# Optimization experiments

Hardware: AMD Instinct MI355X
Metric: run time of the kernel (lower is better)

The kernel has to match this reference:

```python
import jax, jax.numpy as jnp
import numpy as np

NH, NL, NP = 8, 4, 4  # heads, levels, points per head per level
SHAPES = [(100, 134), (50, 67), (25, 34), (13, 17)]  # (H, W) per level, strides 8/16/32/64


def rms_norm(x, w, eps=1e-6):
    return x * jax.lax.rsqrt(jnp.mean(x * x, axis=-1, keepdims=True) + eps) * w


def bilinear_sample(value_l, loc, H, W):
    """grid_sample(bilinear, zeros padding, align_corners=False) equivalent.
    value_l: (bs, nh, H*W, d); loc: (bs, Lq, nh, P, 2) normalized to [0,1].
    Returns (bs, Lq, nh, P, d)."""
    bs, Lq, nh, P, _ = loc.shape
    x = loc[..., 0] * W - 0.5
    y = loc[..., 1] * H - 0.5
    x0 = jnp.floor(x); y0 = jnp.floor(y)
    lx = x - x0; ly = y - y0
    x0i = x0.astype(jnp.int32); y0i = y0.astype(jnp.int32)
    out = None
    for dy, dx in ((0, 0), (0, 1), (1, 0), (1, 1)):
        wgt = (lx if dx else 1.0 - lx) * (ly if dy else 1.0 - ly)
        xi = x0i + dx; yi = y0i + dy
        valid = (xi >= 0) & (xi < W) & (yi >= 0) & (yi < H)
        idx = jnp.clip(yi, 0, H - 1) * W + jnp.clip(xi, 0, W - 1)  # (bs,Lq,nh,P)
        idx_t = idx.transpose(0, 2, 1, 3).reshape(bs, nh, Lq * P)
        g = jnp.take_along_axis(value_l, idx_t[..., None], axis=2)  # (bs,nh,Lq*P,d)
        g = g.reshape(bs, nh, Lq, P, -1).transpose(0, 2, 1, 3, 4)    # (bs,Lq,nh,P,d)
        term = g * (wgt * valid)[..., None]
        out = term if out is None else out + term
    return out


def _forward(query, query_pos, reference_points, norm_attn_w, Wv, bv, Woff, boff, Waw, baw, Wo, bo, ls_attn_g, norm_ffn_w, W1, b1, W2, b2, W3, b3, ls_ffn_g):
    bs, Lq, C = query.shape
    d = C // NH
    # --- pre-norm MSDeformAttn with identity=0 (LayerScale residual applied outside) ---
    normed = rms_norm(query, norm_attn_w)
    q = normed + query_pos  # query_pos only affects offsets/weights, not value
    value = (normed @ Wv.T + bv).reshape(bs, Lq, NH, d).transpose(0, 2, 1, 3)  # (bs,nh,Nv,d)
    off = (q @ Woff.T + boff).reshape(bs, Lq, NH, NL, NP, 2)
    aw = jax.nn.softmax((q @ Waw.T + baw).reshape(bs, Lq, NH, NL * NP), axis=-1)
    aw = aw.reshape(bs, Lq, NH, NL, NP)
    normalizer = jnp.array([[w, h] for (h, w) in SHAPES], dtype=query.dtype)  # (NL,2) = (W,H)
    loc = reference_points[:, :, None, :, None, :] + off / normalizer[None, None, None, :, None, :]
    out = jnp.zeros((bs, Lq, NH, d), query.dtype)
    start = 0
    for l, (H, W) in enumerate(SHAPES):
        v_l = jax.lax.dynamic_slice_in_dim(value, start, H * W, axis=2)
        samp = bilinear_sample(v_l, loc[:, :, :, l], H, W)  # (bs,Lq,nh,P,d)
        out = out + jnp.einsum('bqhpd,bqhp->bqhd', samp, aw[:, :, :, l])
        start += H * W
    attn_out = out.reshape(bs, Lq, C) @ Wo.T + bo
    x = query + ls_attn_g * attn_out
    # --- pre-norm SwiGLU FFN with LayerScale residual ---
    n2 = rms_norm(x, norm_ffn_w)
    h = jax.nn.silu(n2 @ W1.T + b1) * (n2 @ W2.T + b2)
    return x + ls_ffn_g * (h @ W3.T + b3)


def setup_inputs() -> dict:
    key = jax.random.key(0)
    ks = jax.random.split(key, 12)
    bs, C, dffn = 2, 256, 1024
    Lq = sum(h * w for h, w in SHAPES)  # 17821
    p = 0.02
    return {
        'query': jax.random.normal(ks[0], (bs, Lq, C), jnp.float32),
        'query_pos': jax.random.normal(ks[1], (bs, Lq, C), jnp.float32),
        'reference_points': jax.random.uniform(ks[2], (bs, Lq, NL, 2), jnp.float32),
        'spatial_shapes': jnp.array(SHAPES, jnp.int32),
        'level_start_index': jnp.array(np.cumsum([0] + [h * w for h, w in SHAPES])[:-1], jnp.int32),
        'norm_attn_w': jnp.ones((C,), jnp.float32),
        'Wv': jax.random.normal(ks[3], (C, C), jnp.float32) * p,
        'bv': jnp.zeros((C,), jnp.float32),
        'Woff': jax.random.normal(ks[4], (NH * NL * NP * 2, C), jnp.float32) * p,
        'boff': jax.random.uniform(ks[5], (NH * NL * NP * 2,), jnp.float32, -1.0, 1.0),
        'Waw': jax.random.normal(ks[6], (NH * NL * NP, C), jnp.float32) * p,
        'baw': jnp.zeros((NH * NL * NP,), jnp.float32),
        'Wo': jax.random.normal(ks[7], (C, C), jnp.float32) * p,
        'bo': jnp.zeros((C,), jnp.float32),
        'ls_attn_g': jnp.full((C,), 1e-4, jnp.float32),
        'norm_ffn_w': jnp.ones((C,), jnp.float32),
        'W1': jax.random.normal(ks[8], (dffn, C), jnp.float32) * p,
        'b1': jnp.zeros((dffn,), jnp.float32),
        'W2': jax.random.normal(ks[9], (dffn, C), jnp.float32) * p,
        'b2': jnp.zeros((dffn,), jnp.float32),
        'W3': jax.random.normal(ks[10], (C, dffn), jnp.float32) * p,
        'b3': jnp.zeros((C,), jnp.float32),
        'ls_ffn_g': jnp.full((C,), 1e-4, jnp.float32),
    }


def reference(query, query_pos, reference_points, spatial_shapes, level_start_index, norm_attn_w, Wv, bv, Woff, boff, Waw, baw, Wo, bo, ls_attn_g, norm_ffn_w, W1, b1, W2, b2, W3, b3, ls_ffn_g):
    del spatial_shapes, level_start_index  # static shapes baked into SHAPES
    return _forward(query, query_pos, reference_points, norm_attn_w, Wv, bv, Woff, boff, Waw, baw, Wo, bo, ls_attn_g, norm_ffn_w, W1, b1, W2, b2, W3, b3, ls_ffn_g)
```

## Files before the change

### kernel.cpp

```cpp
#include <hip/hip_runtime.h>
#include <hip/hip_bf16.h>
#include <cstddef>

#define LQ   17821
#define BS   2
#define MTOK (BS * LQ)
#define CDIM 256
#define NHD  8
#define DHEAD 32
#define DFFN 1024

typedef short bf16x4 __attribute__((ext_vector_type(4)));
typedef short bf16x8 __attribute__((ext_vector_type(8)));
typedef float f32x4  __attribute__((ext_vector_type(4)));
typedef float f32x2  __attribute__((ext_vector_type(2)));

__device__ __forceinline__ unsigned char fp8_enc(float f) {
#if __has_builtin(__builtin_amdgcn_cvt_pk_fp8_f32)
    return (unsigned char)(__builtin_amdgcn_cvt_pk_fp8_f32(f, f, 0, false) & 0xff);
#else
    unsigned s = (__float_as_uint(f) >> 31) << 7;
    float af = fabsf(f);
    if (af < 0.0078125f) return (unsigned char)s;
    af = fminf(af, 448.f);
    unsigned b = __float_as_uint(af);
    int e = (int)(b >> 23) - 127 + 7;
    unsigned m = (b >> 20) & 7;
    if (b & 0x80000) { m++; if (m == 8) { m = 0; e++; } }
    if (e < 1) return (unsigned char)s;
    if (e > 15) { e = 15; m = 6; }
    return (unsigned char)(s | ((unsigned)e << 3) | m);
#endif
}

__device__ __forceinline__ float fp8_dec_byte(unsigned x) {
    unsigned s = (x >> 7) & 1, e = (x >> 3) & 15, m = x & 7;
    float v = e ? __uint_as_float(((e + 120u) << 23) | (m << 20))
                : (float)m * 0.001953125f;
    return s ? -v : v;
}

template <bool HI>
__device__ __forceinline__ f32x2 fp8_dec2(unsigned d) {
#if __has_builtin(__builtin_amdgcn_cvt_pk_f32_fp8)
    return __builtin_amdgcn_cvt_pk_f32_fp8(d, HI);
#else
    f32x2 r;
    r[0] = fp8_dec_byte((d >> (HI ? 16 : 0)) & 0xff);
    r[1] = fp8_dec_byte((d >> (HI ? 24 : 8)) & 0xff);
    return r;
#endif
}

__device__ __forceinline__ ushort bfpack(float f) {
    __hip_bfloat16 h = (__hip_bfloat16)f;
    return *(ushort*)&h;
}

__device__ __forceinline__ void stage_a8(short* p, uint2 d) {
    const f32x2 p0 = fp8_dec2<false>(d.x), p1 = fp8_dec2<true>(d.x);
    const f32x2 p2 = fp8_dec2<false>(d.y), p3 = fp8_dec2<true>(d.y);
    bf16x4 lo, hi;
    lo[0] = (short)bfpack(p0[0]); lo[1] = (short)bfpack(p0[1]);
    lo[2] = (short)bfpack(p1[0]); lo[3] = (short)bfpack(p1[1]);
    hi[0] = (short)bfpack(p2[0]); hi[1] = (short)bfpack(p2[1]);
    hi[2] = (short)bfpack(p3[0]); hi[3] = (short)bfpack(p3[1]);
    ((bf16x4*)p)[0] = lo;
    ((bf16x4*)p)[1] = hi;
}

struct CastJobs {
    const float* src[7];
    __hip_bfloat16* dst[7];
    const float* colw[7];
    int n[7];
};

__global__ __launch_bounds__(256)
void cast_all(CastJobs j) {
    const int seg = blockIdx.y;
    const int i = blockIdx.x * 256 + threadIdx.x;
    if (i < j.n[seg]) {
        float v = j.src[seg][i];
        if (j.colw[seg]) v *= j.colw[seg][i & 255];
        j.dst[seg][i] = (__hip_bfloat16)v;
    }
}

template <bool ADD_POS>
__global__ __launch_bounds__(256)
void rmsnorm_kernel(const float* __restrict__ x, const float* __restrict__ pos,
                    const float* __restrict__ w,
                    __hip_bfloat16* __restrict__ outN, __hip_bfloat16* __restrict__ outQ) {
    const int tok = blockIdx.x * 4 + (threadIdx.x >> 6);
    if (tok >= MTOK) return;
    const int lane = threadIdx.x & 63;
    const size_t base = (size_t)tok * CDIM + lane * 4;
    const float4 v = *(const float4*)&x[base];
    float ss = v.x * v.x + v.y * v.y + v.z * v.z + v.w * v.w;
#pragma unroll
    for (int m = 1; m < 64; m <<= 1) ss += __shfl_xor(ss, m, 64);
    const float r = rsqrtf(ss * (1.0f / CDIM) + 1e-6f);
    const float4 wv = *(const float4*)&w[lane * 4];
    const float n0 = v.x * r * wv.x, n1 = v.y * r * wv.y;
    const float n2 = v.z * r * wv.z, n3 = v.w * r * wv.w;
    ushort4 o;
    o.x = bfpack(n0); o.y = bfpack(n1); o.z = bfpack(n2); o.w = bfpack(n3);
    *(ushort4*)&outN[base] = o;
    if (ADD_POS) {
        const float4 p = *(const float4*)&pos[base];
        ushort4 q;
        q.x = bfpack(n0 + p.x); q.y = bfpack(n1 + p.y);
        q.z = bfpack(n2 + p.z); q.w = bfpack(n3 + p.w);
        *(ushort4*)&outQ[base] = q;
    }
}

__global__ __launch_bounds__(256)
void rowrms_kernel(const __hip_bfloat16* __restrict__ x, float* __restrict__ r) {
    const int tok = blockIdx.x * 4 + (threadIdx.x >> 6);
    if (tok >= MTOK) return;
    const int lane = threadIdx.x & 63;
    const ushort4 u = *(const ushort4*)&x[(size_t)tok * CDIM + lane * 4];
    const float v0 = __uint_as_float((unsigned)u.x << 16);
    const float v1 = __uint_as_float((unsigned)u.y << 16);
    const float v2 = __uint_as_float((unsigned)u.z << 16);
    const float v3 = __uint_as_float((unsigned)u.w << 16);
    float ss = v0 * v0 + v1 * v1 + v2 * v2 + v3 * v3;
#pragma unroll
    for (int m = 1; m < 64; m <<= 1) ss += __shfl_xor(ss, m, 64);
    if (lane == 0) r[tok] = rsqrtf(ss * (1.0f / CDIM) + 1e-6f);
}

#define GBM 128
#define GBN 128

template <int MODE, int BKT, typename OUTT, bool A8 = false>
__global__ __launch_bounds__(256, 2)
void mfma_gemm(const void* __restrict__ Av,
               const __hip_bfloat16* __restrict__ B1, const float* __restrict__ bias1,
               const float* __restrict__ bias2,
               const float* __restrict__ resid, const __hip_bfloat16* __restrict__ residb,
               const float* __restrict__ ls,
               OUTT* __restrict__ out, int M, int N, int K, int nsw) {
    constexpr int LDKT = BKT + 8;
    constexpr int CH = BKT / 16;
    constexpr int CPR = BKT / 8;

    __shared__ short As[GBM * LDKT];
    __shared__ short Bs[GBN * LDKT];

    const __hip_bfloat16* A = (const __hip_bfloat16*)Av;
    const unsigned char* A8p = (const unsigned char*)Av;

    const int tid = threadIdx.x;
    const int bid = blockIdx.x;
    const int m0 = (bid / nsw) * GBM;
    const int n0 = (bid % nsw) * GBN;
    const int wave = tid >> 6;
    const int lane = tid & 63;
    const int wm = (wave >> 1) * 64;
    const int wn = (wave & 1) * 64;
    const int fr = lane & 15;
    const int fq = lane >> 4;

    f32x4 acc[4][4] = {};

    int srow[CH], skc[CH];
#pragma unroll
    for (int cc = 0; cc < CH; ++cc) {
        const int g = tid + cc * 256;
        srow[cc] = g / CPR;
        skc[cc] = (g % CPR) * 8;
    }
    const uint4 zero4 = make_uint4(0, 0, 0, 0);
    const uint2 zero2 = make_uint2(0, 0);

    uint4 ra[CH], rb[CH];
    uint2 ra8[A8 ? CH : 1];
#pragma unroll
    for (int cc = 0; cc < CH; ++cc) {
        const int gm = m0 + srow[cc];
        if constexpr (A8)
            ra8[cc] = (gm < M) ? *(const uint2*)&A8p[(size_t)gm * K + skc[cc]] : zero2;
        else
            ra[cc] = (gm < M) ? *(const uint4*)&A[(size_t)gm * K + skc[cc]] : zero4;
        rb[cc] = *(const uint4*)&B1[(size_t)(n0 + srow[cc]) * K + skc[cc]];
    }

    for (int k0 = 0; k0 < K; k0 += BKT) {
        __syncthreads();
#pragma unroll
        for (int cc = 0; cc < CH; ++cc) {
            short* pa = &As[srow[cc] * LDKT + skc[cc]];
            short* pb = &Bs[srow[cc] * LDKT + skc[cc]];
            if constexpr (A8) {
                stage_a8(pa, ra8[cc]);
            } else {
                union { uint4 u; bf16x4 h[2]; } cv;
                cv.u = ra[cc]; ((bf16x4*)pa)[0] = cv.h[0]; ((bf16x4*)pa)[1] = cv.h[1];
            }
            union { uint4 u; bf16x4 h[2]; } cv;
            cv.u = rb[cc]; ((bf16x4*)pb)[0] = cv.h[0]; ((bf16x4*)pb)[1] = cv.h[1];
        }
        __syncthreads();

        if (k0 + BKT < K) {
            const int kn = k0 + BKT;
#pragma unroll
            for (int cc = 0; cc < CH; ++cc) {
                const int gm = m0 + srow[cc];
                if constexpr (A8)
                    ra8[cc] = (gm < M) ? *(const uint2*)&A8p[(size_t)gm * K + kn + skc[cc]] : zero2;
                else
                    ra[cc] = (gm < M) ? *(const uint4*)&A[(size_t)gm * K + kn + skc[cc]] : zero4;
                rb[cc] = *(const uint4*)&B1[(size_t)(n0 + srow[cc]) * K + kn + skc[cc]];
            }
        }

#pragma unroll
        for (int kk = 0; kk < BKT; kk += 32) {
            const int kq = kk + fq * 8;
            bf16x8 af[4], bfr[4];
#pragma unroll
            for (int i = 0; i < 4; ++i)
                af[i] = *(const bf16x8*)&As[(wm + i * 16 + fr) * LDKT + kq];
#pragma unroll
            for (int j = 0; j < 4; ++j)
                bfr[j] = *(const bf16x8*)&Bs[(wn + j * 16 + fr) * LDKT + kq];
#pragma unroll
            for (int i = 0; i < 4; ++i)
#pragma unroll
                for (int j = 0; j < 4; ++j)
                    acc[i][j] = __builtin_amdgcn_mfma_f32_16x16x32_bf16(af[i], bfr[j], acc[i][j], 0, 0, 0);
        }
    }

#pragma unroll
    for (int i = 0; i < 4; ++i) {
#pragma unroll
        for (int r = 0; r < 4; ++r) {
            const int m = m0 + wm + i * 16 + fq * 4 + r;
            if (m >= M) continue;
#pragma unroll
            for (int j = 0; j < 4; ++j) {
                const int n = n0 + wn + j * 16 + fr;
                float v;
                if constexpr (MODE == 4)
                    v = acc[i][j][r] + ((n < 256) ? bias1[n] : bias2[n - 256]);
                else
                    v = acc[i][j][r] + bias1[n];
                if constexpr (MODE == 0 || MODE == 4) {
                    out[(size_t)m * N + n] = (OUTT)v;
                } else if constexpr (MODE == 1) {
                    const int b = (m >= LQ) ? 1 : 0;
                    const int qi = m - b * LQ;
                    const int h = n >> 5;
                    const int c = n & 31;
                    ((unsigned char*)out)[((size_t)(b * NHD + h) * LQ + qi) * DHEAD + c] = fp8_enc(v);
                } else if constexpr (MODE == 2) {
                    out[(size_t)m * N + n] =
                        (OUTT)(resid[(size_t)m * N + n] + ls[n] * v);
                } else {
                    const float rx = __uint_as_float(
                        (unsigned)(*(const ushort*)&residb[(size_t)m * N + n]) << 16);
                    out[(size_t)m * N + n] = (OUTT)(rx + ls[n] * v);
                }
            }
        }
    }
}

__global__ __launch_bounds__(256, 3)
void mfma_swiglu(const __hip_bfloat16* __restrict__ A,
                 const __hip_bfloat16* __restrict__ B1, const float* __restrict__ bias1,
                 const __hip_bfloat16* __restrict__ B2, const float* __restrict__ bias2,
                 const float* __restrict__ rrow,
                 unsigned char* __restrict__ out, int M) {
    constexpr int BKT = 32, LDKT = 40, K = CDIM, N = DFFN;
    __shared__ short As[128 * LDKT];
    __shared__ short Bs[64 * LDKT];
    __shared__ short Bs2[64 * LDKT];

    const int tid = threadIdx.x;
    const int bid = blockIdx.x;
    const int m0 = (bid >> 4) * 128;
    const int n0 = (bid & 15) * 64;
    const int wave = tid >> 6;
    const int lane = tid & 63;
    const int wm = (wave >> 1) * 64;
    const int wn = (wave & 1) * 32;
    const int fr = lane & 15;
    const int fq = lane >> 4;

    f32x4 acc[4][2] = {};
    f32x4 acc2[4][2] = {};

    const int arow = tid >> 2;
    const int akc = (tid & 3) * 8;
    const uint4 zero4 = make_uint4(0, 0, 0, 0);

    uint4 ra0, ra1, rb, rc;
    {
        const int gm0 = m0 + arow, gm1 = m0 + arow + 64;
        ra0 = (gm0 < M) ? *(const uint4*)&A[(size_t)gm0 * K + akc] : zero4;
        ra1 = (gm1 < M) ? *(const uint4*)&A[(size_t)gm1 * K + akc] : zero4;
        rb = *(const uint4*)&B1[(size_t)(n0 + arow) * K + akc];
        rc = *(const uint4*)&B2[(size_t)(n0 + arow) * K + akc];
    }

    for (int k0 = 0; k0 < K; k0 += BKT) {
        __syncthreads();
        {
            union { uint4 u; bf16x4 h[2]; } cv;
            short* pa0 = &As[arow * LDKT + akc];
            short* pa1 = &As[(arow + 64) * LDKT + akc];
            short* pb = &Bs[arow * LDKT + akc];
            short* pc = &Bs2[arow * LDKT + akc];
            cv.u = ra0; ((bf16x4*)pa0)[0] = cv.h[0]; ((bf16x4*)pa0)[1] = cv.h[1];
            cv.u = ra1; ((bf16x4*)pa1)[0] = cv.h[0]; ((bf16x4*)pa1)[1] = cv.h[1];
            cv.u = rb;  ((bf16x4*)pb)[0] = cv.h[0]; ((bf16x4*)pb)[1] = cv.h[1];
            cv.u = rc;  ((bf16x4*)pc)[0] = cv.h[0]; ((bf16x4*)pc)[1] = cv.h[1];
        }
        __syncthreads();

        if (k0 + BKT < K) {
            const int kn = k0 + BKT + akc;
            const int gm0 = m0 + arow, gm1 = m0 + arow + 64;
            ra0 = (gm0 < M) ? *(const uint4*)&A[(size_t)gm0 * K + kn] : zero4;
            ra1 = (gm1 < M) ? *(const uint4*)&A[(size_t)gm1 * K + kn] : zero4;
            rb = *(const uint4*)&B1[(size_t)(n0 + arow) * K + kn];
            rc = *(const uint4*)&B2[(size_t)(n0 + arow) * K + kn];
        }

        const int kq = fq * 8;
        bf16x8 af[4], bfr[2], bg[2];
#pragma unroll
        for (int i = 0; i < 4; ++i)
            af[i] = *(const bf16x8*)&As[(wm + i * 16 + fr) * LDKT + kq];
#pragma unroll
        for (int j = 0; j < 2; ++j) {
            bfr[j] = *(const bf16x8*)&Bs[(wn + j * 16 + fr) * LDKT + kq];
            bg[j] = *(const bf16x8*)&Bs2[(wn + j * 16 + fr) * LDKT + kq];
        }
#pragma unroll
        for (int i = 0; i < 4; ++i)
#pragma unroll
            for (int j = 0; j < 2; ++j) {
                acc[i][j] = __builtin_amdgcn_mfma_f32_16x16x32_bf16(af[i], bfr[j], acc[i][j], 0, 0, 0);
                acc2[i][j] = __builtin_amdgcn_mfma_f32_16x16x32_bf16(af[i], bg[j], acc2[i][j], 0, 0, 0);
            }
    }

#pragma unroll
    for (int i = 0; i < 4; ++i) {
#pragma unroll
        for (int r = 0; r < 4; ++r) {
            const int m = m0 + wm + i * 16 + fq * 4 + r;
            if (m >= M) continue;
            const float rm = rrow[m];
#pragma unroll
            for (int j = 0; j < 2; ++j) {
                const int n = n0 + wn + j * 16 + fr;
                const float v1 = acc[i][j][r] * rm + bias1[n];
                const float v2 = acc2[i][j][r] * rm + bias2[n];
                const float sig = 1.0f / (1.0f + expf(-v1));
                out[(size_t)m * N + n] = fp8_enc(v1 * sig * v2);
            }
        }
    }
}

__global__ __launch_bounds__(256)
void sample_kernel(const unsigned char* __restrict__ value,
                   const ushort* __restrict__ proj,
                   const float* __restrict__ ref,
                   __hip_bfloat16* __restrict__ out) {
    __shared__ float wsm[4][NHD][16];
    __shared__ int2  sTap[4][64][9];

    const int tok0 = blockIdx.x * 4;
    const int t = threadIdx.x;

    if (t < 32) {
        const int tl = t >> 3, h = t & 7;
        const int row = tok0 + tl;
        if (row < MTOK) {
            const ushort* lg = &proj[(size_t)row * 384 + 256 + h * 16];
            float v[16];
            float mx = -3.4e38f;
#pragma unroll
            for (int i = 0; i < 16; ++i) {
                v[i] = __uint_as_float((unsigned)lg[i] << 16);
                mx = fmaxf(mx, v[i]);
            }
            float s = 0.f;
#pragma unroll
            for (int i = 0; i < 16; ++i) { v[i] = expf(v[i] - mx); s += v[i]; }
            const float inv = 1.0f / s;
#pragma unroll
            for (int i = 0; i < 16; ++i) wsm[tl][h][i] = v[i] * inv;
        }
    }
    __syncthreads();

#pragma unroll
    for (int e = t; e < 512; e += 256) {
        const int tl = e >> 7, hp = e & 127;
        const int row = tok0 + tl;
        if (row < MTOK) {
            const int h = hp >> 4, pt = hp & 15, lv = pt >> 2;
            const int Hs[4] = {100, 50, 25, 13};
            const int Ws[4] = {134, 67, 34, 17};
            const int stt[4] = {0, 13400, 16750, 17600};
            const int H = Hs[lv], W = Ws[lv];
            const float rx = ref[((size_t)row * 4 + lv) * 2 + 0];
            const float ry = ref[((size_t)row * 4 + lv) * 2 + 1];
            const float ox = __uint_as_float((unsigned)proj[(size_t)row * 384 + h * 32 + pt * 2 + 0] << 16);
            const float oy = __uint_as_float((unsigned)proj[(size_t)row * 384 + h * 32 + pt * 2 + 1] << 16);
            const float xf = rx * (float)W + ox - 0.5f;
            const float yf = ry * (float)H + oy - 0.5f;
            const float x0f = floorf(xf), y0f = floorf(yf);
            const float fx = xf - x0f, fy = yf - y0f;
            const int x0 = (int)x0f, y0 = (int)y0f;
            const float aw = wsm[tl][h][pt];
            const int b = (row >= LQ) ? 1 : 0;
            const int base = (b * NHD + h) * LQ + stt[lv];
#pragma unroll
            for (int tap = 0; tap < 4; ++tap) {
                const int dy = tap >> 1, dx = tap & 1;
                const int xi = x0 + dx, yi = y0 + dy;
                const bool valid = (xi >= 0) & (xi < W) & (yi >= 0) & (yi < H);
                const float wgt = (dx ? fx : 1.f - fx) * (dy ? fy : 1.f - fy) * aw;
                sTap[tl][pt * 4 + tap][h] = valid
                    ? make_int2((base + yi * W + xi) * DHEAD, __float_as_int(wgt))
                    : make_int2(0, 0);
            }
        }
    }
    __syncthreads();

    const int tl = t >> 6, lane = t & 63;
    const int row = tok0 + tl;
    if (row >= MTOK) return;
    const int h = lane >> 3, c0 = (lane & 7) * 4;
    const unsigned char* vb = value + c0;
    float a0 = 0.f, a1 = 0.f, a2 = 0.f, a3 = 0.f;
#pragma unroll 8
    for (int i = 0; i < 64; ++i) {
        const int2 tp = sTap[tl][i][h];
        const float w = __int_as_float(tp.y);
        const unsigned d = *(const unsigned*)(vb + (size_t)tp.x);
        const f32x2 lo = fp8_dec2<false>(d);
        const f32x2 hi = fp8_dec2<true>(d);
        a0 = fmaf(w, lo[0], a0);
        a1 = fmaf(w, lo[1], a1);
        a2 = fmaf(w, hi[0], a2);
        a3 = fmaf(w, hi[1], a3);
    }
    ushort4 o;
    o.x = bfpack(a0); o.y = bfpack(a1); o.z = bfpack(a2); o.w = bfpack(a3);
    *(ushort4*)&out[(size_t)row * 256 + h * 32 + c0] = o;
}

extern "C" void kernel_launch(void* const* d_in, const int* in_sizes, int n_in,
                              void* d_out, int out_size, void* d_ws, size_t ws_size,
                              hipStream_t stream) {
    const float* query      = (const float*)d_in[0];
    const float* query_pos  = (const float*)d_in[1];
    const float* ref        = (const float*)d_in[2];
    const float* norm_attn_w = (const float*)d_in[5];
    const float* Wv   = (const float*)d_in[6];
    const float* bv   = (const float*)d_in[7];
    const float* Woff = (const float*)d_in[8];
    const float* boff = (const float*)d_in[9];
    const float* Waw  = (const float*)d_in[10];
    const float* baw  = (const float*)d_in[11];
    const float* Wo   = (const float*)d_in[12];
    const float* bo   = (const float*)d_in[13];
    const float* ls_attn = (const float*)d_in[14];
    const float* norm_ffn_w = (const float*)d_in[15];
    const float* W1 = (const float*)d_in[16];
    const float* b1 = (const float*)d_in[17];
    const float* W2 = (const float*)d_in[18];
    const float* b2 = (const float*)d_in[19];
    const float* W3 = (const float*)d_in[20];
    const float* b3 = (const float*)d_in[21];
    const float* ls_ffn = (const float*)d_in[22];
    float* out = (float*)d_out;

    char* ws = (char*)d_ws;
    const size_t MCb = (size_t)MTOK * CDIM * 2;

    __hip_bfloat16* normed_bf  = (__hip_bfloat16*)(ws);
    __hip_bfloat16* q_bf       = (__hip_bfloat16*)(ws + MCb);
    unsigned char*  value_u8   = (unsigned char*)(ws + 2 * MCb);
    __hip_bfloat16* proj_bf    = (__hip_bfloat16*)(ws + 3 * MCb);
    __hip_bfloat16* sampled_bf = (__hip_bfloat16*)(ws);
    __hip_bfloat16* x_bf       = (__hip_bfloat16*)(ws + MCb);
    float*          r_f        = (float*)(ws + 2 * MCb);
    unsigned char*  h_u8       = (unsigned char*)(ws + 3 * MCb);
    __hip_bfloat16* wbf        = (__hip_bfloat16*)(ws + 7 * MCb);

    __hip_bfloat16* Wv_bf    = wbf;
    __hip_bfloat16* Wproj_bf = wbf + 65536;
    __hip_bfloat16* Wo_bf    = wbf + 163840;
    __hip_bfloat16* W1_bf    = wbf + 229376;
    __hip_bfloat16* W2_bf    = wbf + 491520;
    __hip_bfloat16* W3_bf    = wbf + 753664;

    CastJobs cj;
    cj.src[0] = Wv;   cj.dst[0] = Wv_bf;            cj.colw[0] = nullptr; cj.n[0] = 65536;
    cj.src[1] = Woff; cj.dst[1] = Wproj_bf;         cj.colw[1] = nullptr; cj.n[1] = 65536;
    cj.src[2] = Waw;  cj.dst[2] = Wproj_bf + 65536; cj.colw[2] = nullptr; cj.n[2] = 32768;
    cj.src[3] = Wo;   cj.dst[3] = Wo_bf;            cj.colw[3] = nullptr; cj.n[3] = 65536;
    cj.src[4] = W1;   cj.dst[4] = W1_bf;            cj.colw[4] = norm_ffn_w; cj.n[4] = 262144;
    cj.src[5] = W2;   cj.dst[5] = W2_bf;            cj.colw[5] = norm_ffn_w; cj.n[5] = 262144;
    cj.src[6] = W3;   cj.dst[6] = W3_bf;            cj.colw[6] = nullptr; cj.n[6] = 262144;
    cast_all<<<dim3(1024, 7), 256, 0, stream>>>(cj);

    const int gx = (MTOK + GBM - 1) / GBM;
    const int gr = (MTOK + 3) / 4;

    rmsnorm_kernel<true><<<gr, 256, 0, stream>>>(query, query_pos, norm_attn_w, normed_bf, q_bf);
    mfma_gemm<1, 64, unsigned char><<<gx * 2, 256, 0, stream>>>(
        normed_bf, Wv_bf, bv, nullptr, nullptr, nullptr, nullptr, value_u8, MTOK, CDIM, CDIM, 2);
    mfma_gemm<4, 64, __hip_bfloat16><<<gx * 3, 256, 0, stream>>>(
        q_bf, Wproj_bf, boff, baw, nullptr, nullptr, nullptr, proj_bf, MTOK, 384, CDIM, 3);
    sample_kernel<<<gr, 256, 0, stream>>>(value_u8, (const ushort*)proj_bf, ref, sampled_bf);
    mfma_gemm<2, 64, __hip_bfloat16><<<gx * 2, 256, 0, stream>>>(
        sampled_bf, Wo_bf, bo, nullptr, query, nullptr, ls_attn, x_bf, MTOK, CDIM, CDIM, 2);
    rowrms_kernel<<<gr, 256, 0, stream>>>(x_bf, r_f);
    mfma_swiglu<<<gx * 16, 256, 0, stream>>>(
        x_bf, W1_bf, b1, W2_bf, b2, r_f, h_u8, MTOK);
    mfma_gemm<5, 64, float, true><<<gx * 2, 256, 0, stream>>>(
        h_u8, W3_bf, b3, nullptr, nullptr, x_bf, ls_ffn, out, MTOK, CDIM, DFFN, 2);
}
```

Before: 389.6 us.

## Interleave W1/W2 rows and run SwiGLU through generic MFMA GEMM epilogue

The W1 and W2 weights are cast into one interleaved matrix with rows alternating between them. The dedicated dual-accumulator SwiGLU kernel is replaced by the generic MFMA GEMM with N=2048 and a new epilogue mode. In that mode adjacent columns are paired through a lane shuffle, and the even lane applies the row RMS scale, the biases, the sigmoid gate and the fp8 store. This drops the dual-B staging and reuses the generic kernel's tiling, at the cost of twice as many output columns per tile and half the lanes idle in the store. The softmax also switches from expf to __expf.

New measurement: 453.6 us. 16.4% more time.

```diff
diff --git a/kernel.cpp b/kernel.cpp
--- a/kernel.cpp
+++ b/kernel.cpp
@@ -74,6 +74,8 @@
     __hip_bfloat16* dst[7];
     const float* colw[7];
     int n[7];
+    int rmul[7];
+    int radd[7];
 };
 
 __global__ __launch_bounds__(256)
@@ -83,7 +85,8 @@
     if (i < j.n[seg]) {
         float v = j.src[seg][i];
         if (j.colw[seg]) v *= j.colw[seg][i & 255];
-        j.dst[seg][i] = (__hip_bfloat16)v;
+        const size_t di = ((size_t)(i >> 8) * j.rmul[seg] + j.radd[seg]) * 256 + (i & 255);
+        j.dst[seg][di] = (__hip_bfloat16)v;
     }
 }
 
@@ -248,6 +251,8 @@
                 float v;
                 if constexpr (MODE == 4)
                     v = acc[i][j][r] + ((n < 256) ? bias1[n] : bias2[n - 256]);
+                else if constexpr (MODE == 6)
+                    v = acc[i][j][r] * resid[m] + ((n & 1) ? bias2[n >> 1] : bias1[n >> 1]);
                 else
                     v = acc[i][j][r] + bias1[n];
                 if constexpr (MODE == 0 || MODE == 4) {
@@ -261,111 +266,18 @@
                 } else if constexpr (MODE == 2) {
                     out[(size_t)m * N + n] =
                         (OUTT)(resid[(size_t)m * N + n] + ls[n] * v);
+                } else if constexpr (MODE == 6) {
+                    const float other = __shfl_xor(v, 1, 64);
+                    if (!(lane & 1)) {
+                        const float sig = 1.0f / (1.0f + __expf(-v));
+                        ((unsigned char*)out)[(size_t)m * (N >> 1) + (n >> 1)] =
+                            fp8_enc(v * sig * other);
+                    }
                 } else {
                     const float rx = __uint_as_float(
                         (unsigned)(*(const ushort*)&residb[(size_t)m * N + n]) << 16);
                     out[(size_t)m * N + n] = (OUTT)(rx + ls[n] * v);
                 }
-            }
-        }
-    }
-}
-
-__global__ __launch_bounds__(256, 3)
-void mfma_swiglu(const __hip_bfloat16* __restrict__ A,
-                 const __hip_bfloat16* __restrict__ B1, const float* __restrict__ bias1,
-                 const __hip_bfloat16* __restrict__ B2, const float* __restrict__ bias2,
-                 const float* __restrict__ rrow,
-                 unsigned char* __restrict__ out, int M) {
-    constexpr int BKT = 32, LDKT = 40, K = CDIM, N = DFFN;
-    __shared__ short As[128 * LDKT];
-    __shared__ short Bs[64 * LDKT];
-    __shared__ short Bs2[64 * LDKT];
-
-    const int tid = threadIdx.x;
-    const int bid = blockIdx.x;
-    const int m0 = (bid >> 4) * 128;
-    const int n0 = (bid & 15) * 64;
-    const int wave = tid >> 6;
-    const int lane = tid & 63;
-    const int wm = (wave >> 1) * 64;
-    const int wn = (wave & 1) * 32;
-    const int fr = lane & 15;
-    const int fq = lane >> 4;
-
-    f32x4 acc[4][2] = {};
-    f32x4 acc2[4][2] = {};
-
-    const int arow = tid >> 2;
-    const int akc = (tid & 3) * 8;
-    const uint4 zero4 = make_uint4(0, 0, 0, 0);
-
-    uint4 ra0, ra1, rb, rc;
-    {
-        const int gm0 = m0 + arow, gm1 = m0 + arow + 64;
-        ra0 = (gm0 < M) ? *(const uint4*)&A[(size_t)gm0 * K + akc] : zero4;
-        ra1 = (gm1 < M) ? *(const uint4*)&A[(size_t)gm1 * K + akc] : zero4;
-        rb = *(const uint4*)&B1[(size_t)(n0 + arow) * K + akc];
-        rc = *(const uint4*)&B2[(size_t)(n0 + arow) * K + akc];
-    }
-
-    for (int k0 = 0; k0 < K; k0 += BKT) {
-        __syncthreads();
-        {
-            union { uint4 u; bf16x4 h[2]; } cv;
-            short* pa0 = &As[arow * LDKT + akc];
-            short* pa1 = &As[(arow + 64) * LDKT + akc];
-            short* pb = &Bs[arow * LDKT + akc];
-            short* pc = &Bs2[arow * LDKT + akc];
-            cv.u = ra0; ((bf16x4*)pa0)[0] = cv.h[0]; ((bf16x4*)pa0)[1] = cv.h[1];
-            cv.u = ra1; ((bf16x4*)pa1)[0] = cv.h[0]; ((bf16x4*)pa1)[1] = cv.h[1];
-            cv.u = rb;  ((bf16x4*)pb)[0] = cv.h[0]; ((bf16x4*)pb)[1] = cv.h[1];
-            cv.u = rc;  ((bf16x4*)pc)[0] = cv.h[0]; ((bf16x4*)pc)[1] = cv.h[1];
-        }
-        __syncthreads();
-
-        if (k0 + BKT < K) {
-            const int kn = k0 + BKT + akc;
-            const int gm0 = m0 + arow, gm1 = m0 + arow + 64;
-            ra0 = (gm0 < M) ? *(const uint4*)&A[(size_t)gm0 * K + kn] : zero4;
-            ra1 = (gm1 < M) ? *(const uint4*)&A[(size_t)gm1 * K + kn] : zero4;
-            rb = *(const uint4*)&B1[(size_t)(n0 + arow) * K + kn];
-            rc = *(const uint4*)&B2[(size_t)(n0 + arow) * K + kn];
-        }
-
-        const int kq = fq * 8;
-        bf16x8 af[4], bfr[2], bg[2];
-#pragma unroll
-        for (int i = 0; i < 4; ++i)
-            af[i] = *(const bf16x8*)&As[(wm + i * 16 + fr) * LDKT + kq];
-#pragma unroll
-        for (int j = 0; j < 2; ++j) {
-            bfr[j] = *(const bf16x8*)&Bs[(wn + j * 16 + fr) * LDKT + kq];
-            bg[j] = *(const bf16x8*)&Bs2[(wn + j * 16 + fr) * LDKT + kq];
-        }
-#pragma unroll
-        for (int i = 0; i < 4; ++i)
-#pragma unroll
-            for (int j = 0; j < 2; ++j) {
-                acc[i][j] = __builtin_amdgcn_mfma_f32_16x16x32_bf16(af[i], bfr[j], acc[i][j], 0, 0, 0);
-                acc2[i][j] = __builtin_amdgcn_mfma_f32_16x16x32_bf16(af[i], bg[j], acc2[i][j], 0, 0, 0);
-            }
-    }
-
-#pragma unroll
-    for (int i = 0; i < 4; ++i) {
-#pragma unroll
-        for (int r = 0; r < 4; ++r) {
-            const int m = m0 + wm + i * 16 + fq * 4 + r;
-            if (m >= M) continue;
-            const float rm = rrow[m];
-#pragma unroll
-            for (int j = 0; j < 2; ++j) {
-                const int n = n0 + wn + j * 16 + fr;
-                const float v1 = acc[i][j][r] * rm + bias1[n];
-                const float v2 = acc2[i][j][r] * rm + bias2[n];
-                const float sig = 1.0f / (1.0f + expf(-v1));
-                out[(size_t)m * N + n] = fp8_enc(v1 * sig * v2);
             }
         }
     }
@@ -396,7 +308,7 @@
             }
             float s = 0.f;
 #pragma unroll
-            for (int i = 0; i < 16; ++i) { v[i] = expf(v[i] - mx); s += v[i]; }
+            for (int i = 0; i < 16; ++i) { v[i] = __expf(v[i] - mx); s += v[i]; }
             const float inv = 1.0f / s;
 #pragma unroll
             for (int i = 0; i < 16; ++i) wsm[tl][h][i] = v[i] * inv;
@@ -505,18 +417,17 @@
     __hip_bfloat16* Wv_bf    = wbf;
     __hip_bfloat16* Wproj_bf = wbf + 65536;
     __hip_bfloat16* Wo_bf    = wbf + 163840;
-    __hip_bfloat16* W1_bf    = wbf + 229376;
-    __hip_bfloat16* W2_bf    = wbf + 491520;
+    __hip_bfloat16* Wcat_bf  = wbf + 229376;
     __hip_bfloat16* W3_bf    = wbf + 753664;
 
     CastJobs cj;
-    cj.src[0] = Wv;   cj.dst[0] = Wv_bf;            cj.colw[0] = nullptr; cj.n[0] = 65536;
-    cj.src[1] = Woff; cj.dst[1] = Wproj_bf;         cj.colw[1] = nullptr; cj.n[1] = 65536;
-    cj.src[2] = Waw;  cj.dst[2] = Wproj_bf + 65536; cj.colw[2] = nullptr; cj.n[2] = 32768;
-    cj.src[3] = Wo;   cj.dst[3] = Wo_bf;            cj.colw[3] = nullptr; cj.n[3] = 65536;
-    cj.src[4] = W1;   cj.dst[4] = W1_bf;            cj.colw[4] = norm_ffn_w; cj.n[4] = 262144;
-    cj.src[5] = W2;   cj.dst[5] = W2_bf;            cj.colw[5] = norm_ffn_w; cj.n[5] = 262144;
-    cj.src[6] = W3;   cj.dst[6] = W3_bf;            cj.colw[6] = nullptr; cj.n[6] = 262144;
+    cj.src[0] = Wv;   cj.dst[0] = Wv_bf;            cj.colw[0] = nullptr; cj.n[0] = 65536;  cj.rmul[0] = 1; cj.radd[0] = 0;
+    cj.src[1] = Woff; cj.dst[1] = Wproj_bf;         cj.colw[1] = nullptr; cj.n[1] = 65536;  cj.rmul[1] = 1; cj.radd[1] = 0;
+    cj.src[2] = Waw;  cj.dst[2] = Wproj_bf + 65536; cj.colw[2] = nullptr; cj.n[2] = 32768;  cj.rmul[2] = 1; cj.radd[2] = 0;
+    cj.src[3] = Wo;   cj.dst[3] = Wo_bf;            cj.colw[3] = nullptr; cj.n[3] = 65536;  cj.rmul[3] = 1; cj.radd[3] = 0;
+    cj.src[4] = W1;   cj.dst[4] = Wcat_bf;          cj.colw[4] = norm_ffn_w; cj.n[4] = 262144; cj.rmul[4] = 2; cj.radd[4] = 0;
+    cj.src[5] = W2;   cj.dst[5] = Wcat_bf;          cj.colw[5] = norm_ffn_w; cj.n[5] = 262144; cj.rmul[5] = 2; cj.radd[5] = 1;
+    cj.src[6] = W3;   cj.dst[6] = W3_bf;            cj.colw[6] = nullptr; cj.n[6] = 262144; cj.rmul[6] = 1; cj.radd[6] = 0;
     cast_all<<<dim3(1024, 7), 256, 0, stream>>>(cj);
 
     const int gx = (MTOK + GBM - 1) / GBM;
@@ -531,8 +442,8 @@
     mfma_gemm<2, 64, __hip_bfloat16><<<gx * 2, 256, 0, stream>>>(
         sampled_bf, Wo_bf, bo, nullptr, query, nullptr, ls_attn, x_bf, MTOK, CDIM, CDIM, 2);
     rowrms_kernel<<<gr, 256, 0, stream>>>(x_bf, r_f);
-    mfma_swiglu<<<gx * 16, 256, 0, stream>>>(
-        x_bf, W1_bf, b1, W2_bf, b2, r_f, h_u8, MTOK);
+    mfma_gemm<6, 64, unsigned char><<<gx * 16, 256, 0, stream>>>(
+        x_bf, Wcat_bf, b1, b2, r_f, nullptr, nullptr, h_u8, MTOK, 2048, CDIM, 16);
     mfma_gemm<5, 64, float, true><<<gx * 2, 256, 0, stream>>>(
         h_u8, W3_bf, b3, nullptr, nullptr, x_bf, ls_ffn, out, MTOK, CDIM, DFFN, 2);
 }
```
